# Optimization experiments

Measured on AMD Instinct MI355X. Metric: run time of the kernel, lower is better.

Reference implementation:

```python
import jax, jax.numpy as jnp
import numpy as np

H = 128      # hidden_dim
N = 200000   # number of available (job, machine) ops
M = 1000     # machine nodes
J = 5000     # job nodes


def setup_inputs() -> dict:
    key = jax.random.key(0)
    ks = jax.random.split(key, 8)
    s = 0.05  # weight scale
    return {
        "x_graph": jax.random.normal(ks[0], (1, 2 * H), jnp.float32),
        "x_m": jax.random.normal(ks[1], (M, H), jnp.float32),
        "x_job": jax.random.normal(ks[2], (J, H), jnp.float32),
        "m_ids": jax.random.randint(ks[3], (N,), 0, M),
        "job_idx": jax.random.randint(ks[4], (N,), 0, J),
        "W0": jax.random.normal(ks[5], (4 * H, H), jnp.float32) * s,
        "b0": jnp.zeros((H,), jnp.float32),
        "W1": jax.random.normal(ks[6], (H, H), jnp.float32) * s,
        "b1": jnp.zeros((H,), jnp.float32),
        "W2": jax.random.normal(ks[7], (H, 1), jnp.float32) * s,
        "b2": jnp.zeros((1,), jnp.float32),
    }


def reference(x_graph, x_m, x_job, m_ids, job_idx, W0, b0, W1, b1, W2, b2):
    n = m_ids.shape[0]
    # vectorized form of the python loop: [x_graph | x_m[m_id] | x_job[job_pos]] -> [N, 4H]
    feats = jnp.concatenate(
        [
            jnp.broadcast_to(x_graph, (n, x_graph.shape[1])),
            x_m[m_ids],
            x_job[job_idx],
        ],
        axis=1,
    )
    h = jax.nn.relu(feats @ W0 + b0)   # Linear(4H -> H) + ReLU
    h = jax.nn.relu(h @ W1 + b1)       # Linear(H -> H) + ReLU
    scores = (h @ W2 + b2)[:, 0]       # Linear(H -> 1), squeeze -> [N]
    logp = jax.nn.log_softmax(scores, axis=0)
    probs = jnp.exp(logp)
    idx = jnp.argmax(scores)           # greedy selection (deterministic baseline)
    entropy = -jnp.sum(probs * logp)   # Categorical entropy
    return idx, probs[idx], logp[idx], entropy
```

## Files before the change

kernel.cpp:

```cpp
#include <hip/hip_runtime.h>
#include <math.h>

#define HID 128
#define TILE_R 64
#define TILE_P 32
#define XS_STRIDE 132
#define H0S_STRIDE 136
#define DELTA 0.05f
#define MAIN_GRID 1024

typedef short bf16x8 __attribute__((ext_vector_type(8)));
typedef float f32x4 __attribute__((ext_vector_type(4)));

static __device__ __forceinline__ unsigned short f2bf(float f) {
    union { float f; unsigned u; } v; v.f = f;
    unsigned r = v.u + 0x7FFFu + ((v.u >> 16) & 1u);
    return (unsigned short)(r >> 16);
}
static __device__ __forceinline__ float bflo(unsigned u) {
    union { unsigned u; float f; } v; v.u = u << 16; return v.f;
}
static __device__ __forceinline__ float bfhi(unsigned u) {
    union { unsigned u; float f; } v; v.u = u & 0xFFFF0000u; return v.f;
}

#define FMA4(avc, wv)                         \
    acc[r][0] = fmaf(avc, wv.x, acc[r][0]);   \
    acc[r][1] = fmaf(avc, wv.y, acc[r][1]);   \
    acc[r][2] = fmaf(avc, wv.z, acc[r][2]);   \
    acc[r][3] = fmaf(avc, wv.w, acc[r][3]);

__global__ __launch_bounds__(256, 4) void precompute_kernel(
    const float* __restrict__ x_graph,
    const float* __restrict__ x_m,
    const float* __restrict__ x_job,
    const float* __restrict__ W0,
    const float* __restrict__ b0,
    const float* __restrict__ W1,
    float* __restrict__ g,
    unsigned short* __restrict__ Pbf,
    unsigned short* __restrict__ W1T,
    int M, int J, int aTiles, int bTiles)
{
    const int t = threadIdx.x;
    const int bid = blockIdx.x;

    if (bid == 0) {
        __shared__ float xg[2 * HID];
        if (t < HID) { xg[t] = x_graph[t]; xg[t + HID] = x_graph[t + HID]; }
        __syncthreads();
        if (t < HID) {
            float acc = b0[t];
            #pragma unroll 8
            for (int k = 0; k < 2 * HID; ++k)
                acc = fmaf(xg[k], W0[k * HID + t], acc);
            g[t] = acc;
        }
        return;
    }
    if (bid == 1 + aTiles + bTiles) {
        for (int e = t; e < HID * HID; e += 256) {
            int n = e >> 7, k = e & 127;
            W1T[e] = f2bf(W1[k * HID + n]);
        }
        return;
    }

    const int tb = bid - 1;
    const float* X;
    const float* W;
    int r0, nr, dstBase;
    if (tb < aTiles) {
        r0 = tb * TILE_P;
        nr = min(TILE_P, M - r0);
        X = x_m + (size_t)r0 * HID;
        W = W0 + 2 * HID * HID;
        dstBase = r0;
    } else {
        int jb = tb - aTiles;
        r0 = jb * TILE_P;
        nr = min(TILE_P, J - r0);
        X = x_job + (size_t)r0 * HID;
        W = W0 + 3 * HID * HID;
        dstBase = M + r0;
    }

    __shared__ float xs[TILE_P * XS_STRIDE];
    {
        int row = t >> 3;
        int e = t & 7;
        #pragma unroll
        for (int u = 0; u < 4; ++u) {
            int c = e * 16 + u * 4;
            float4 v = (row < nr) ? *(const float4*)(X + row * HID + c)
                                  : make_float4(0.f, 0.f, 0.f, 0.f);
            *(float4*)&xs[row * XS_STRIDE + c] = v;
        }
    }
    __syncthreads();

    const int w = t >> 6;
    const int l = t & 63;
    const int tc = l & 7;
    const int tr = l >> 3;
    const int c0 = w * 32 + tc * 4;

    float acc[4][4];
    #pragma unroll
    for (int r = 0; r < 4; ++r)
        #pragma unroll
        for (int c = 0; c < 4; ++c) acc[r][c] = 0.0f;

    #pragma unroll 2
    for (int k0 = 0; k0 < HID; k0 += 4) {
        float4 w0v = *(const float4*)(W + (k0 + 0) * HID + c0);
        float4 w1v = *(const float4*)(W + (k0 + 1) * HID + c0);
        float4 w2m = *(const float4*)(W + (k0 + 2) * HID + c0);
        float4 w3v = *(const float4*)(W + (k0 + 3) * HID + c0);
        #pragma unroll
        for (int r = 0; r < 4; ++r) {
            float4 a = *(const float4*)&xs[(r * 8 + tr) * XS_STRIDE + k0];
            FMA4(a.x, w0v)
            FMA4(a.y, w1v)
            FMA4(a.z, w2m)
            FMA4(a.w, w3v)
        }
    }

    #pragma unroll
    for (int r = 0; r < 4; ++r) {
        int row = r * 8 + tr;
        if (row < nr) {
            unsigned lo0 = (unsigned)f2bf(acc[r][0]) | ((unsigned)f2bf(acc[r][1]) << 16);
            unsigned lo1 = (unsigned)f2bf(acc[r][2]) | ((unsigned)f2bf(acc[r][3]) << 16);
            uint2 pk = make_uint2(lo0, lo1);
            *(uint2*)(Pbf + (size_t)(dstBase + row) * HID + c0) = pk;
        }
    }
}

__global__ __launch_bounds__(256, 4) void main_kernel(
    const int* __restrict__ m_ids,
    const int* __restrict__ job_idx,
    const float* __restrict__ b1,
    const float* __restrict__ W2,
    const float* __restrict__ b2,
    const float* __restrict__ g,
    const unsigned short* __restrict__ Pbf,
    const unsigned short* __restrict__ W1T,
    float* __restrict__ scores,
    float4* __restrict__ partials,
    float* __restrict__ tmax,
    int N, int M, int tiles)
{
    __shared__ __align__(16) short h0s[TILE_R * H0S_STRIDE];
    __shared__ float sred[4 * TILE_R];

    const int t = threadIdx.x;
    const int l = t & 63;
    const int w = t >> 6;
    const int quad = l >> 4;
    const int mrow = l & 15;

    bf16x8 bfr[2][4];
    {
        const unsigned short* wb = W1T + (size_t)(w * 32 + mrow) * HID + quad * 8;
        #pragma unroll
        for (int nt = 0; nt < 2; ++nt)
            #pragma unroll
            for (int kc = 0; kc < 4; ++kc)
                bfr[nt][kc] = *(const bf16x8*)(wb + nt * 16 * HID + kc * 32);
    }
    const float b1v0 = b1[w * 32 + mrow];
    const float b1v1 = b1[w * 32 + 16 + mrow];
    const float w2v0 = W2[w * 32 + mrow];
    const float w2v1 = W2[w * 32 + 16 + mrow];
    const float b2v = b2[0];

    for (int tile = blockIdx.x; tile < tiles; tile += MAIN_GRID) {
        const int row0 = tile * TILE_R;

        {
            int row = t >> 2;
            int q = t & 3;
            int grow = row0 + row;
            int gr = (grow < N) ? grow : (N - 1);
            int m = m_ids[gr];
            int j = job_idx[gr];
            const unsigned short* pm = Pbf + (size_t)m * HID + q * 32;
            const unsigned short* pj = Pbf + (size_t)(M + j) * HID + q * 32;
            const float* gp = g + q * 32;
            short* dst = &h0s[row * H0S_STRIDE + q * 32];
            #pragma unroll
            for (int u = 0; u < 4; ++u) {
                uint4 mv = *(const uint4*)(pm + u * 8);
                uint4 jv = *(const uint4*)(pj + u * 8);
                float4 g0 = *(const float4*)(gp + u * 8);
                float4 g1 = *(const float4*)(gp + u * 8 + 4);
                float h0v = fmaxf(bflo(mv.x) + bflo(jv.x) + g0.x, 0.f);
                float h1v = fmaxf(bfhi(mv.x) + bfhi(jv.x) + g0.y, 0.f);
                float h2v = fmaxf(bflo(mv.y) + bflo(jv.y) + g0.z, 0.f);
                float h3v = fmaxf(bfhi(mv.y) + bfhi(jv.y) + g0.w, 0.f);
                float h4v = fmaxf(bflo(mv.z) + bflo(jv.z) + g1.x, 0.f);
                float h5v = fmaxf(bfhi(mv.z) + bfhi(jv.z) + g1.y, 0.f);
                float h6v = fmaxf(bflo(mv.w) + bflo(jv.w) + g1.z, 0.f);
                float h7v = fmaxf(bfhi(mv.w) + bfhi(jv.w) + g1.w, 0.f);
                uint4 pk;
                pk.x = (unsigned)f2bf(h0v) | ((unsigned)f2bf(h1v) << 16);
                pk.y = (unsigned)f2bf(h2v) | ((unsigned)f2bf(h3v) << 16);
                pk.z = (unsigned)f2bf(h4v) | ((unsigned)f2bf(h5v) << 16);
                pk.w = (unsigned)f2bf(h6v) | ((unsigned)f2bf(h7v) << 16);
                *(uint4*)(dst + u * 8) = pk;
            }
        }
        __syncthreads();

        f32x4 acc[4][2];
        #pragma unroll
        for (int mt = 0; mt < 4; ++mt) {
            f32x4 z = {0.f, 0.f, 0.f, 0.f};
            acc[mt][0] = z;
            acc[mt][1] = z;
        }
        #pragma unroll
        for (int mt = 0; mt < 4; ++mt) {
            const short* ab = &h0s[(mt * 16 + mrow) * H0S_STRIDE + quad * 8];
            #pragma unroll
            for (int kc = 0; kc < 4; ++kc) {
                bf16x8 af = *(const bf16x8*)(ab + kc * 32);
                acc[mt][0] = __builtin_amdgcn_mfma_f32_16x16x32_bf16(af, bfr[0][kc], acc[mt][0], 0, 0, 0);
                acc[mt][1] = __builtin_amdgcn_mfma_f32_16x16x32_bf16(af, bfr[1][kc], acc[mt][1], 0, 0, 0);
            }
        }

        #pragma unroll
        for (int mt = 0; mt < 4; ++mt) {
            float p[4];
            #pragma unroll
            for (int i = 0; i < 4; ++i) {
                p[i] = fmaxf(acc[mt][0][i] + b1v0, 0.f) * w2v0
                     + fmaxf(acc[mt][1][i] + b1v1, 0.f) * w2v1;
            }
            #pragma unroll
            for (int off = 1; off < 16; off <<= 1) {
                #pragma unroll
                for (int i = 0; i < 4; ++i)
                    p[i] += __shfl_xor(p[i], off);
            }
            if (mrow == 0) {
                int rb = mt * 16 + quad * 4;
                sred[w * TILE_R + rb + 0] = p[0];
                sred[w * TILE_R + rb + 1] = p[1];
                sred[w * TILE_R + rb + 2] = p[2];
                sred[w * TILE_R + rb + 3] = p[3];
            }
        }
        __syncthreads();

        if (t < 64) {
            int grow = row0 + t;
            float s = sred[t] + sred[64 + t] + sred[128 + t] + sred[192 + t] + b2v;
            if (grow < N) scores[grow] = s;
            else s = -1e30f;

            float mmax = s;
            int midx = grow;
            #pragma unroll
            for (int off = 1; off < 64; off <<= 1) {
                float om = __shfl_xor(mmax, off);
                int oi = __shfl_xor(midx, off);
                if (om > mmax || (om == mmax && oi < midx)) { mmax = om; midx = oi; }
            }
            float d = s - mmax;
            float e = expf(d);
            float z = e;
            float ss = d * e;
            #pragma unroll
            for (int off = 1; off < 64; off <<= 1) {
                z += __shfl_xor(z, off);
                ss += __shfl_xor(ss, off);
            }
            if (t == 0) {
                partials[tile] = make_float4(mmax, z, ss, (float)midx);
                tmax[tile] = mmax;
            }
        }
    }
}

__device__ inline void sm_merge(float& am, float& az, float& ass, int& ai,
                                float bm, float bz, float bss, int bi)
{
    if (bm > am || (bm == am && bi < ai)) {
        float tm = am, tz = az, ts = ass; int ti = ai;
        am = bm; az = bz; ass = bss; ai = bi;
        bm = tm; bz = tz; bss = ts; bi = ti;
    }
    float f = expf(bm - am);
    az += bz * f;
    ass += (bss + (bm - am) * bz) * f;
}

__global__ __launch_bounds__(256) void scan_kernel(
    const float* __restrict__ tmax, int nparts,
    const float* __restrict__ scores,
    const int* __restrict__ m_ids,
    const int* __restrict__ job_idx,
    const float* __restrict__ x_m,
    const float* __restrict__ x_job,
    const float* __restrict__ W0,
    const float* __restrict__ W1,
    const float* __restrict__ b1,
    const float* __restrict__ W2,
    const float* __restrict__ b2,
    const float* __restrict__ g,
    float2* __restrict__ bests,
    int N)
{
    __shared__ int cand[256];
    __shared__ int ccount;
    __shared__ float rs[4];
    __shared__ int ri[4];
    __shared__ float mmx[4];

    const int t = threadIdx.x;
    const int w = t >> 6;
    const int l = t & 63;
    const int base = blockIdx.x * 256;

    float m0 = -1e30f, m1 = -1e30f, m2 = -1e30f, m3 = -1e30f;
    int i = t;
    for (; i + 768 < nparts; i += 1024) {
        m0 = fmaxf(m0, tmax[i]);
        m1 = fmaxf(m1, tmax[i + 256]);
        m2 = fmaxf(m2, tmax[i + 512]);
        m3 = fmaxf(m3, tmax[i + 768]);
    }
    for (; i < nparts; i += 256) m0 = fmaxf(m0, tmax[i]);
    float mhat = fmaxf(fmaxf(m0, m1), fmaxf(m2, m3));
    #pragma unroll
    for (int off = 1; off < 64; off <<= 1)
        mhat = fmaxf(mhat, __shfl_xor(mhat, off));
    if (l == 0) mmx[w] = mhat;
    if (t == 0) ccount = 0;
    __syncthreads();
    mhat = fmaxf(fmaxf(mmx[0], mmx[1]), fmaxf(mmx[2], mmx[3]));
    const float cut = mhat - DELTA;

    int idx = base + t;
    if (idx < N && scores[idx] >= cut) {
        int p = atomicAdd(&ccount, 1);
        cand[p] = idx;
    }
    __syncthreads();
    const int nc = ccount;
    if (nc == 0) {
        if (t == 0) bests[blockIdx.x] = make_float2(-1e30f, __int_as_float(0x7fffffff));
        return;
    }

    float bs = -1e30f;
    int bi = 0x7fffffff;
    for (int c = w; c < nc; c += 4) {
        int gr = cand[c];
        int mm = m_ids[gr];
        int jj = job_idx[gr];
        const float* xm = x_m + (size_t)mm * HID;
        const float* xj = x_job + (size_t)jj * HID;
        const float* wm = W0 + 2 * HID * HID;
        const float* wj = W0 + 3 * HID * HID;
        float a0 = g[l], a1 = g[l + 64];
        for (int k = 0; k < HID; ++k) {
            float xmk = xm[k];
            float xjk = xj[k];
            a0 = fmaf(xmk, wm[k * HID + l], a0);
            a1 = fmaf(xmk, wm[k * HID + l + 64], a1);
            a0 = fmaf(xjk, wj[k * HID + l], a0);
            a1 = fmaf(xjk, wj[k * HID + l + 64], a1);
        }
        a0 = fmaxf(a0, 0.f);
        a1 = fmaxf(a1, 0.f);
        float acc0 = 0.f, acc1 = 0.f;
        for (int k = 0; k < 64; ++k) {
            float h = __shfl(a0, k);
            acc0 = fmaf(h, W1[k * HID + l], acc0);
            acc1 = fmaf(h, W1[k * HID + l + 64], acc1);
        }
        for (int k = 0; k < 64; ++k) {
            float h = __shfl(a1, k);
            acc0 = fmaf(h, W1[(k + 64) * HID + l], acc0);
            acc1 = fmaf(h, W1[(k + 64) * HID + l + 64], acc1);
        }
        float p = fmaxf(acc0 + b1[l], 0.f) * W2[l]
                + fmaxf(acc1 + b1[l + 64], 0.f) * W2[l + 64];
        #pragma unroll
        for (int off = 1; off < 64; off <<= 1)
            p += __shfl_xor(p, off);
        float s = p + b2[0];
        if (s > bs || (s == bs && gr < bi)) { bs = s; bi = gr; }
    }
    if (l == 0) { rs[w] = bs; ri[w] = bi; }
    __syncthreads();
    if (t == 0) {
        float best = rs[0];
        int bwin = ri[0];
        for (int i2 = 1; i2 < 4; ++i2)
            if (rs[i2] > best || (rs[i2] == best && ri[i2] < bwin)) {
                best = rs[i2]; bwin = ri[i2];
            }
        bests[blockIdx.x] = make_float2(best, __int_as_float(bwin));
    }
}

__global__ __launch_bounds__(256) void finalize_kernel(
    const float4* __restrict__ partials, int nparts,
    const float2* __restrict__ bests, int nblocks,
    float* __restrict__ out)
{
    __shared__ float4 wred[4];
    __shared__ int widx[4];
    __shared__ float rs[4];
    __shared__ int ri[4];
    const int t = threadIdx.x;
    const int w = t >> 6;
    const int l = t & 63;

    float m = -1e30f, z = 0.f, ss = 0.f;
    int idx = 0x7fffffff;
    for (int i = t; i < nparts; i += 256) {
        float4 p = partials[i];
        sm_merge(m, z, ss, idx, p.x, p.y, p.z, (int)p.w);
    }
    #pragma unroll
    for (int off = 1; off < 64; off <<= 1) {
        float om = __shfl_xor(m, off);
        float oz = __shfl_xor(z, off);
        float os = __shfl_xor(ss, off);
        int oi = __shfl_xor(idx, off);
        sm_merge(m, z, ss, idx, om, oz, os, oi);
    }
    if (l == 0) { wred[w] = make_float4(m, z, ss, 0.f); widx[w] = idx; }

    float bs = -1e30f;
    int bi = 0x7fffffff;
    for (int i = t; i < nblocks; i += 256) {
        float2 b = bests[i];
        int gi = __float_as_int(b.y);
        if (b.x > bs || (b.x == bs && gi < bi)) { bs = b.x; bi = gi; }
    }
    #pragma unroll
    for (int off = 1; off < 64; off <<= 1) {
        float os = __shfl_xor(bs, off);
        int oi = __shfl_xor(bi, off);
        if (os > bs || (os == bs && oi < bi)) { bs = os; bi = oi; }
    }
    if (l == 0) { rs[w] = bs; ri[w] = bi; }
    __syncthreads();

    if (t == 0) {
        for (int i = 1; i < 4; ++i) {
            sm_merge(m, z, ss, idx, wred[i].x, wred[i].y, wred[i].z, widx[i]);
            if (rs[i] > bs || (rs[i] == bs && ri[i] < bi)) { bs = rs[i]; bi = ri[i]; }
        }
        float logZ = logf(z);
        out[0] = (float)bi;
        out[1] = expf(bs - m) / z;
        out[2] = (bs - m) - logZ;
        out[3] = logZ - ss / z;
    }
}

extern "C" void kernel_launch(void* const* d_in, const int* in_sizes, int n_in,
                              void* d_out, int out_size, void* d_ws, size_t ws_size,
                              hipStream_t stream)
{
    const float* x_graph = (const float*)d_in[0];
    const float* x_m     = (const float*)d_in[1];
    const float* x_job   = (const float*)d_in[2];
    const int*   m_ids   = (const int*)d_in[3];
    const int*   job_idx = (const int*)d_in[4];
    const float* W0      = (const float*)d_in[5];
    const float* b0      = (const float*)d_in[6];
    const float* W1      = (const float*)d_in[7];
    const float* b1      = (const float*)d_in[8];
    const float* W2      = (const float*)d_in[9];
    const float* b2      = (const float*)d_in[10];
    float* out = (float*)d_out;

    const int N = in_sizes[3];
    const int M = in_sizes[1] / HID;
    const int J = in_sizes[2] / HID;

    const int tiles = (N + TILE_R - 1) / TILE_R;
    const int aTiles = (M + TILE_P - 1) / TILE_P;
    const int bTiles = (J + TILE_P - 1) / TILE_P;
    const int sblocks = (N + 255) / 256;

    float* ws = (float*)d_ws;
    float* g = ws;
    float* scores = ws + HID;
    float4* partials = (float4*)(scores + N);
    float* tmax = (float*)(partials + tiles);
    const int tmaxPad = (tiles + 3) & ~3;
    float2* bests = (float2*)(tmax + tmaxPad);
    unsigned short* W1T = (unsigned short*)(bests + sblocks + (sblocks & 1));
    unsigned short* Pbf = W1T + HID * HID;

    precompute_kernel<<<1 + aTiles + bTiles + 1, 256, 0, stream>>>(
        x_graph, x_m, x_job, W0, b0, W1, g, Pbf, W1T, M, J, aTiles, bTiles);
    main_kernel<<<MAIN_GRID, 256, 0, stream>>>(
        m_ids, job_idx, b1, W2, b2, g, Pbf, W1T, scores, partials, tmax,
        N, M, tiles);
    scan_kernel<<<sblocks, 256, 0, stream>>>(
        tmax, tiles, scores, m_ids, job_idx, x_m, x_job, W0, W1, b1, W2, b2,
        g, bests, N);
    finalize_kernel<<<1, 256, 0, stream>>>(partials, tiles, bests, sblocks, out);
}
```

Measured before the change: 139.7 us.

## Collect near-max candidates in main kernel and fold rescoring into finalize

The main kernel no longer writes a full scores array. Each block keeps a running max and appends rows within DELTA of it to a shared list, then flushes that list to a global candidate buffer with one atomic per block. The separate scan kernel is removed, and the single-block finalize filters candidates against the global max and rescores them in fp32. This saves one launch and the N-wide score write and reread, but the fixed caps (LCAP, GCAP) could overflow on adversarial score distributions, and the exact rescoring now runs serially in one block.

```diff
diff --git a/kernel.cpp b/kernel.cpp
--- a/kernel.cpp
+++ b/kernel.cpp
@@ -8,6 +8,8 @@
 #define H0S_STRIDE 136
 #define DELTA 0.05f
 #define MAIN_GRID 1024
+#define LCAP 128
+#define GCAP 8192
 
 typedef short bf16x8 __attribute__((ext_vector_type(8)));
 typedef float f32x4 __attribute__((ext_vector_type(4)));
@@ -40,12 +42,14 @@
     float* __restrict__ g,
     unsigned short* __restrict__ Pbf,
     unsigned short* __restrict__ W1T,
+    int* __restrict__ ncand,
     int M, int J, int aTiles, int bTiles)
 {
     const int t = threadIdx.x;
     const int bid = blockIdx.x;
 
     if (bid == 0) {
+        if (t == 0) *ncand = 0;
         __shared__ float xg[2 * HID];
         if (t < HID) { xg[t] = x_graph[t]; xg[t + HID] = x_graph[t + HID]; }
         __syncthreads();
@@ -148,13 +152,17 @@
     const float* __restrict__ g,
     const unsigned short* __restrict__ Pbf,
     const unsigned short* __restrict__ W1T,
-    float* __restrict__ scores,
     float4* __restrict__ partials,
-    float* __restrict__ tmax,
+    int* __restrict__ candIdx,
+    float* __restrict__ candS,
+    int* __restrict__ ncand,
     int N, int M, int tiles)
 {
     __shared__ __align__(16) short h0s[TILE_R * H0S_STRIDE];
     __shared__ float sred[4 * TILE_R];
+    __shared__ int lcand[LCAP];
+    __shared__ float lcs[LCAP];
+    __shared__ int lcnt;
 
     const int t = threadIdx.x;
     const int l = t & 63;
@@ -162,6 +170,8 @@
     const int quad = l >> 4;
     const int mrow = l & 15;
 
+    if (t == 0) lcnt = 0;
+
     bf16x8 bfr[2][4];
     {
         const unsigned short* wb = W1T + (size_t)(w * 32 + mrow) * HID + quad * 8;
@@ -176,6 +186,8 @@
     const float w2v0 = W2[w * 32 + mrow];
     const float w2v1 = W2[w * 32 + 16 + mrow];
     const float b2v = b2[0];
+
+    float rmax = -1e30f;
 
     for (int tile = blockIdx.x; tile < tiles; tile += MAIN_GRID) {
         const int row0 = tile * TILE_R;
@@ -259,9 +271,9 @@
 
         if (t < 64) {
             int grow = row0 + t;
+            bool valid = grow < N;
             float s = sred[t] + sred[64 + t] + sred[128 + t] + sred[192 + t] + b2v;
-            if (grow < N) scores[grow] = s;
-            else s = -1e30f;
+            if (!valid) s = -1e30f;
 
             float mmax = s;
             int midx = grow;
@@ -280,9 +292,33 @@
                 z += __shfl_xor(z, off);
                 ss += __shfl_xor(ss, off);
             }
-            if (t == 0) {
-                partials[tile] = make_float4(mmax, z, ss, (float)midx);
-                tmax[tile] = mmax;
+            if (t == 0) partials[tile] = make_float4(mmax, z, ss, (float)midx);
+
+            rmax = fmaxf(rmax, mmax);
+            unsigned long long qm = __ballot(valid && (s >= rmax - DELTA));
+            if (qm) {
+                int cnt = __popcll(qm);
+                int rank = __popcll(qm & ((1ull << t) - 1ull));
+                int lb;
+                if (t == 0) lb = atomicAdd(&lcnt, cnt);
+                lb = __shfl(lb, 0);
+                if ((qm >> t) & 1ull) {
+                    int p = lb + rank;
+                    if (p < LCAP) { lcand[p] = grow; lcs[p] = s; }
+                }
+            }
+        }
+    }
+
+    if (t < 64) {
+        int cnt = min(lcnt, LCAP);
+        if (cnt > 0) {
+            int gb;
+            if (t == 0) gb = atomicAdd(ncand, cnt);
+            gb = __shfl(gb, 0);
+            for (int c = t; c < cnt; c += 64) {
+                int p = gb + c;
+                if (p < GCAP) { candIdx[p] = lcand[c]; candS[p] = lcs[c]; }
             }
         }
     }
@@ -301,9 +337,11 @@
     ass += (bss + (bm - am) * bz) * f;
 }
 
-__global__ __launch_bounds__(256) void scan_kernel(
-    const float* __restrict__ tmax, int nparts,
-    const float* __restrict__ scores,
+__global__ __launch_bounds__(256) void finalize_kernel(
+    const float4* __restrict__ partials, int nparts,
+    const int* __restrict__ candIdx,
+    const float* __restrict__ candS,
+    const int* __restrict__ ncand,
     const int* __restrict__ m_ids,
     const int* __restrict__ job_idx,
     const float* __restrict__ x_m,
@@ -314,55 +352,55 @@
     const float* __restrict__ W2,
     const float* __restrict__ b2,
     const float* __restrict__ g,
-    float2* __restrict__ bests,
+    float* __restrict__ out,
     int N)
 {
-    __shared__ int cand[256];
-    __shared__ int ccount;
+    __shared__ float4 wred[4];
+    __shared__ int widx[4];
+    __shared__ int surv[LCAP];
+    __shared__ int scnt;
     __shared__ float rs[4];
     __shared__ int ri[4];
-    __shared__ float mmx[4];
 
     const int t = threadIdx.x;
     const int w = t >> 6;
     const int l = t & 63;
-    const int base = blockIdx.x * 256;
-
-    float m0 = -1e30f, m1 = -1e30f, m2 = -1e30f, m3 = -1e30f;
-    int i = t;
-    for (; i + 768 < nparts; i += 1024) {
-        m0 = fmaxf(m0, tmax[i]);
-        m1 = fmaxf(m1, tmax[i + 256]);
-        m2 = fmaxf(m2, tmax[i + 512]);
-        m3 = fmaxf(m3, tmax[i + 768]);
-    }
-    for (; i < nparts; i += 256) m0 = fmaxf(m0, tmax[i]);
-    float mhat = fmaxf(fmaxf(m0, m1), fmaxf(m2, m3));
+
+    float m = -1e30f, z = 0.f, ss = 0.f;
+    int idx = 0x7fffffff;
+    for (int i = t; i < nparts; i += 256) {
+        float4 p = partials[i];
+        sm_merge(m, z, ss, idx, p.x, p.y, p.z, (int)p.w);
+    }
     #pragma unroll
-    for (int off = 1; off < 64; off <<= 1)
-        mhat = fmaxf(mhat, __shfl_xor(mhat, off));
-    if (l == 0) mmx[w] = mhat;
-    if (t == 0) ccount = 0;
+    for (int off = 1; off < 64; off <<= 1) {
+        float om = __shfl_xor(m, off);
+        float oz = __shfl_xor(z, off);
+        float os = __shfl_xor(ss, off);
+        int oi = __shfl_xor(idx, off);
+        sm_merge(m, z, ss, idx, om, oz, os, oi);
+    }
+    if (l == 0) { wred[w] = make_float4(m, z, ss, 0.f); widx[w] = idx; }
+    if (t == 0) scnt = 0;
     __syncthreads();
-    mhat = fmaxf(fmaxf(mmx[0], mmx[1]), fmaxf(mmx[2], mmx[3]));
-    const float cut = mhat - DELTA;
-
-    int idx = base + t;
-    if (idx < N && scores[idx] >= cut) {
-        int p = atomicAdd(&ccount, 1);
-        cand[p] = idx;
+
+    const float gm = fmaxf(fmaxf(wred[0].x, wred[1].x), fmaxf(wred[2].x, wred[3].x));
+    const float cut = gm - DELTA;
+
+    const int nc = min(*ncand, GCAP);
+    for (int c = t; c < nc; c += 256) {
+        if (candS[c] >= cut) {
+            int p = atomicAdd(&scnt, 1);
+            if (p < LCAP) surv[p] = candIdx[c];
+        }
     }
     __syncthreads();
-    const int nc = ccount;
-    if (nc == 0) {
-        if (t == 0) bests[blockIdx.x] = make_float2(-1e30f, __int_as_float(0x7fffffff));
-        return;
-    }
+    const int ns = min(scnt, LCAP);
 
     float bs = -1e30f;
     int bi = 0x7fffffff;
-    for (int c = w; c < nc; c += 4) {
-        int gr = cand[c];
+    for (int c = w; c < ns; c += 4) {
+        int gr = surv[c];
         int mm = m_ids[gr];
         int jj = job_idx[gr];
         const float* xm = x_m + (size_t)mm * HID;
@@ -401,67 +439,12 @@
     }
     if (l == 0) { rs[w] = bs; ri[w] = bi; }
     __syncthreads();
+
     if (t == 0) {
-        float best = rs[0];
-        int bwin = ri[0];
-        for (int i2 = 1; i2 < 4; ++i2)
-            if (rs[i2] > best || (rs[i2] == best && ri[i2] < bwin)) {
-                best = rs[i2]; bwin = ri[i2];
-            }
-        bests[blockIdx.x] = make_float2(best, __int_as_float(bwin));
-    }
-}
-
-__global__ __launch_bounds__(256) void finalize_kernel(
-    const float4* __restrict__ partials, int nparts,
-    const float2* __restrict__ bests, int nblocks,
-    float* __restrict__ out)
-{
-    __shared__ float4 wred[4];
-    __shared__ int widx[4];
-    __shared__ float rs[4];
-    __shared__ int ri[4];
-    const int t = threadIdx.x;
-    const int w = t >> 6;
-    const int l = t & 63;
-
-    float m = -1e30f, z = 0.f, ss = 0.f;
-    int idx = 0x7fffffff;
-    for (int i = t; i < nparts; i += 256) {
-        float4 p = partials[i];
-        sm_merge(m, z, ss, idx, p.x, p.y, p.z, (int)p.w);
-    }
-    #pragma unroll
-    for (int off = 1; off < 64; off <<= 1) {
-        float om = __shfl_xor(m, off);
-        float oz = __shfl_xor(z, off);
-        float os = __shfl_xor(ss, off);
-        int oi = __shfl_xor(idx, off);
-        sm_merge(m, z, ss, idx, om, oz, os, oi);
-    }
-    if (l == 0) { wred[w] = make_float4(m, z, ss, 0.f); widx[w] = idx; }
-
-    float bs = -1e30f;
-    int bi = 0x7fffffff;
-    for (int i = t; i < nblocks; i += 256) {
-        float2 b = bests[i];
-        int gi = __float_as_int(b.y);
-        if (b.x > bs || (b.x == bs && gi < bi)) { bs = b.x; bi = gi; }
-    }
-    #pragma unroll
-    for (int off = 1; off < 64; off <<= 1) {
-        float os = __shfl_xor(bs, off);
-        int oi = __shfl_xor(bi, off);
-        if (os > bs || (os == bs && oi < bi)) { bs = os; bi = oi; }
-    }
-    if (l == 0) { rs[w] = bs; ri[w] = bi; }
-    __syncthreads();
-
-    if (t == 0) {
-        for (int i = 1; i < 4; ++i) {
+        for (int i = 1; i < 4; ++i)
             sm_merge(m, z, ss, idx, wred[i].x, wred[i].y, wred[i].z, widx[i]);
+        for (int i = 1; i < 4; ++i)
             if (rs[i] > bs || (rs[i] == bs && ri[i] < bi)) { bs = rs[i]; bi = ri[i]; }
-        }
         float logZ = logf(z);
         out[0] = (float)bi;
         out[1] = expf(bs - m) / z;
@@ -494,25 +477,22 @@
     const int tiles = (N + TILE_R - 1) / TILE_R;
     const int aTiles = (M + TILE_P - 1) / TILE_P;
     const int bTiles = (J + TILE_P - 1) / TILE_P;
-    const int sblocks = (N + 255) / 256;
 
     float* ws = (float*)d_ws;
     float* g = ws;
-    float* scores = ws + HID;
-    float4* partials = (float4*)(scores + N);
-    float* tmax = (float*)(partials + tiles);
-    const int tmaxPad = (tiles + 3) & ~3;
-    float2* bests = (float2*)(tmax + tmaxPad);
-    unsigned short* W1T = (unsigned short*)(bests + sblocks + (sblocks & 1));
+    float4* partials = (float4*)(g + HID);
+    int* candIdx = (int*)(partials + tiles);
+    float* candS = (float*)(candIdx + GCAP);
+    int* ncand = (int*)(candS + GCAP);
+    unsigned short* W1T = (unsigned short*)(ncand + 4);
     unsigned short* Pbf = W1T + HID * HID;
 
     precompute_kernel<<<1 + aTiles + bTiles + 1, 256, 0, stream>>>(
-        x_graph, x_m, x_job, W0, b0, W1, g, Pbf, W1T, M, J, aTiles, bTiles);
+        x_graph, x_m, x_job, W0, b0, W1, g, Pbf, W1T, ncand, M, J, aTiles, bTiles);
     main_kernel<<<MAIN_GRID, 256, 0, stream>>>(
-        m_ids, job_idx, b1, W2, b2, g, Pbf, W1T, scores, partials, tmax,
-        N, M, tiles);
-    scan_kernel<<<sblocks, 256, 0, stream>>>(
-        tmax, tiles, scores, m_ids, job_idx, x_m, x_job, W0, W1, b1, W2, b2,
-        g, bests, N);
-    finalize_kernel<<<1, 256, 0, stream>>>(partials, tiles, bests, sblocks, out);
-}
+        m_ids, job_idx, b1, W2, b2, g, Pbf, W1T, partials,
+        candIdx, candS, ncand, N, M, tiles);
+    finalize_kernel<<<1, 256, 0, stream>>>(
+        partials, tiles, candIdx, candS, ncand, m_ids, job_idx, x_m, x_job,
+        W0, W1, b1, W2, b2, g, out, N);
+}
```

After: 167.5 us. +19.9%, slower.
